# Performance work log

Measured on AMD Instinct MI355X. Metric: run time of the kernel, lower is better.

The kernel has to match this reference:

```python
import jax, jax.numpy as jnp
import numpy as np

D_MODEL = 1024
D_FF = 2048
NUM_EXPERTS = 16
TOP_K = 2
CAPACITY_FACTOR = 1.25
BATCH, SEQ = 4, 2048


def setup_inputs() -> dict:
    key = jax.random.key(0)
    k0, k1, k2, k3 = jax.random.split(key, 4)
    x = jax.random.normal(k0, (BATCH, SEQ, D_MODEL), jnp.float32)
    gate_w = jax.random.normal(k1, (NUM_EXPERTS, D_MODEL), jnp.float32) / np.float32(np.sqrt(D_MODEL))
    w1 = jax.random.normal(k2, (NUM_EXPERTS, D_MODEL, D_FF), jnp.float32) / np.float32(np.sqrt(D_MODEL))
    w2 = jax.random.normal(k3, (NUM_EXPERTS, D_FF, D_MODEL), jnp.float32) / np.float32(np.sqrt(D_FF))
    return {"x": x, "gate_w": gate_w, "w1": w1, "w2": w2}


def reference(x, gate_w, w1, w2):
    B, S, d = x.shape
    T = B * S
    E, K = NUM_EXPERTS, TOP_K
    capacity = int(CAPACITY_FACTOR * T * K / E)  # static

    xf = x.reshape(T, d)                                  # [T, d]
    logits = xf @ gate_w.T                                # [T, E]
    probs = jax.nn.sigmoid(logits)
    top_vals, sel = jax.lax.top_k(probs, K)               # [T, K]
    weights = top_vals / (top_vals.sum(-1, keepdims=True) + 1e-6)

    # Capacity-based ranking: rank of each (token, slot) within its expert,
    # in flattened token-major order (matches torch cumsum over one-hot).
    flat_sel = sel.reshape(-1)                            # [T*K]
    onehot = jax.nn.one_hot(flat_sel, E, dtype=jnp.int32)
    ranks = jnp.take_along_axis(jnp.cumsum(onehot, axis=0), flat_sel[:, None], axis=1)[:, 0] - 1
    valid = ranks < capacity                              # [T*K]

    sentinel = E * capacity
    slot = jnp.where(valid, flat_sel * capacity + ranks, sentinel)

    # token-major repeat matches x_flat.unsqueeze(1).expand(-1,K,-1).reshape(-1,d)
    x_rep = jnp.repeat(xf, K, axis=0)                     # [T*K, d]
    padded = jnp.zeros((sentinel + 1, d), xf.dtype).at[slot].set(x_rep)
    padded = padded[:sentinel].reshape(E, capacity, d)    # [E, C, d]

    h = jax.nn.gelu(jnp.einsum('ecd,edf->ecf', padded, w1), approximate=False)
    out_padded = jnp.einsum('ecf,efd->ecd', h, w2).reshape(sentinel, d)

    gathered = out_padded[jnp.minimum(slot, sentinel - 1)]
    gathered = jnp.where(valid[:, None], gathered, jnp.zeros((), xf.dtype))
    out = (gathered * weights.reshape(-1)[:, None]).reshape(T, K, d).sum(axis=1)
    return out.reshape(B, S, d)
```

## Files before the change

kernel.cpp:

```cpp
#include <hip/hip_runtime.h>
#include <math.h>

#define T_TOK 8192
#define DM 1024
#define DF 2048
#define NE 16
#define TK 2
#define CAP 1280

typedef __bf16 bf16x8 __attribute__((ext_vector_type(8)));
typedef float f32x4 __attribute__((ext_vector_type(4)));

__device__ __forceinline__ unsigned short f2bf(float f) {
  unsigned int u = __float_as_uint(f);
  unsigned int r = (u + 0x7fffu + ((u >> 16) & 1u)) >> 16;
  return (unsigned short)r;
}

__device__ __forceinline__ void async_copy16(const void* g, void* l) {
  __builtin_amdgcn_global_load_lds(
      (const __attribute__((address_space(1))) void*)g,
      (__attribute__((address_space(3))) void*)l, 16, 0, 0);
}

__global__ __launch_bounds__(256) void transpose_conv_kernel(
    const float* __restrict__ in, unsigned short* __restrict__ out, int R, int Cc) {
  __shared__ float tl[32][33];
  size_t eoff = (size_t)blockIdx.z * R * Cc;
  in += eoff; out += eoff;
  int c0 = blockIdx.x * 32, r0 = blockIdx.y * 32;
  int tx = threadIdx.x, ty = threadIdx.y;
#pragma unroll
  for (int r = 0; r < 4; r++)
    tl[ty + r * 8][tx] = in[(size_t)(r0 + ty + r * 8) * Cc + c0 + tx];
  __syncthreads();
#pragma unroll
  for (int r = 0; r < 4; r++)
    out[(size_t)(c0 + ty + r * 8) * R + r0 + tx] = f2bf(tl[tx][ty + r * 8]);
}

__global__ __launch_bounds__(64) void gate_kernel(
    const float* __restrict__ x, const float* __restrict__ gw,
    int* __restrict__ sel, float* __restrict__ wts) {
  int t = blockIdx.x;
  int lane = threadIdx.x;
  const float* xr = x + (size_t)t * DM;
  float acc[NE];
#pragma unroll
  for (int e = 0; e < NE; e++) acc[e] = 0.f;
  for (int j = 0; j < DM / 64; j++) {
    float xv = xr[j * 64 + lane];
#pragma unroll
    for (int e = 0; e < NE; e++) acc[e] += xv * gw[e * DM + j * 64 + lane];
  }
#pragma unroll
  for (int e = 0; e < NE; e++) {
    float v = acc[e];
#pragma unroll
    for (int off = 32; off > 0; off >>= 1) v += __shfl_xor(v, off);
    acc[e] = v;
  }
  if (lane == 0) {
    float p[NE];
#pragma unroll
    for (int e = 0; e < NE; e++) p[e] = 1.f / (1.f + expf(-acc[e]));
    int i0 = 0;
#pragma unroll
    for (int e = 1; e < NE; e++) if (p[e] > p[i0]) i0 = e;
    int i1 = (i0 == 0) ? 1 : 0;
#pragma unroll
    for (int e = 0; e < NE; e++) if (e != i0 && p[e] > p[i1]) i1 = e;
    float v0 = p[i0], v1 = p[i1], s = v0 + v1 + 1e-6f;
    sel[2 * t] = i0; sel[2 * t + 1] = i1;
    wts[2 * t] = v0 / s; wts[2 * t + 1] = v1 / s;
  }
}

__global__ __launch_bounds__(256) void scan_kernel(
    const int* __restrict__ sel, int* __restrict__ pos_slot,
    int* __restrict__ exp_tok, int* __restrict__ counts) {
  int e = blockIdx.x;
  __shared__ int wsum[4];
  int tid = threadIdx.x, lane = tid & 63, wv = tid >> 6;
  int base = 0;
  for (int p0 = 0; p0 < T_TOK * TK; p0 += 256) {
    int p = p0 + tid;
    int flag = (sel[p] == e) ? 1 : 0;
    unsigned long long b = __ballot(flag);
    int pre = __popcll(b & ((1ull << lane) - 1ull));
    if (lane == 0) wsum[wv] = __popcll(b);
    __syncthreads();
    int wbase = 0;
#pragma unroll
    for (int i = 0; i < 4; i++) if (i < wv) wbase += wsum[i];
    int tot = wsum[0] + wsum[1] + wsum[2] + wsum[3];
    if (flag) {
      int rank = base + wbase + pre;
      if (rank < CAP) {
        pos_slot[p] = e * CAP + rank;
        exp_tok[e * CAP + rank] = p;
      } else {
        pos_slot[p] = -1;
      }
    }
    base += tot;
    __syncthreads();
  }
  if (tid == 0) counts[e] = base < CAP ? base : CAP;
}

__global__ __launch_bounds__(128) void gather_kernel(
    const float* __restrict__ x, const int* __restrict__ exp_tok,
    const int* __restrict__ counts, unsigned short* __restrict__ Xp) {
  int i = blockIdx.x, e = blockIdx.y;
  int tid = threadIdx.x;
  unsigned short* dst = Xp + ((size_t)e * CAP + i) * DM;
  int4 pk = make_int4(0, 0, 0, 0);
  if (i < counts[e]) {
    int p = exp_tok[e * CAP + i];
    int t = p >> 1;
    const float4* src = (const float4*)(x + (size_t)t * DM);
    float4 v0 = src[tid * 2];
    float4 v1 = src[tid * 2 + 1];
    union { unsigned short u[8]; int4 v; } q;
    q.u[0] = f2bf(v0.x); q.u[1] = f2bf(v0.y); q.u[2] = f2bf(v0.z); q.u[3] = f2bf(v0.w);
    q.u[4] = f2bf(v1.x); q.u[5] = f2bf(v1.y); q.u[6] = f2bf(v1.z); q.u[7] = f2bf(v1.w);
    pk = q.v;
  }
  ((int4*)dst)[tid] = pk;
}

__device__ __forceinline__ void storev(unsigned short* p, float v) { *p = f2bf(v); }
__device__ __forceinline__ void storev(float* p, float v) { *p = v; }

template <bool GELU, typename OutT>
__global__ __launch_bounds__(256) void gemm_bt_kernel(
    const unsigned short* __restrict__ A, const unsigned short* __restrict__ Bt,
    OutT* __restrict__ C, int M, int N, int K,
    size_t sA, size_t sB, size_t sC) {
  __shared__ unsigned short As[128 * 32];
  __shared__ unsigned short Bs[128 * 32];
  A += (size_t)blockIdx.z * sA;
  Bt += (size_t)blockIdx.z * sB;
  C += (size_t)blockIdx.z * sC;
  int m0 = blockIdx.y * 128, n0 = blockIdx.x * 128;
  int tid = threadIdx.x;
  int lane = tid & 63;
  int wv = tid >> 6;
  int wm = (wv >> 1) * 64, wn = (wv & 1) * 64;
  int qd = lane >> 4, lm = lane & 15;

  const unsigned short* a0 = A + (size_t)(m0 + (tid >> 2)) * K + (tid & 3) * 8;
  const unsigned short* a1 = a0 + (size_t)64 * K;
  const unsigned short* b0 = Bt + (size_t)(n0 + (tid >> 2)) * K + (tid & 3) * 8;
  const unsigned short* b1 = b0 + (size_t)64 * K;
  char* lAs = (char*)As;
  char* lBs = (char*)Bs;

  f32x4 acc[4][4] = {};
  for (int k0 = 0; k0 < K; k0 += 32) {
    __syncthreads();
    async_copy16(a0 + k0, lAs + tid * 16);
    async_copy16(a1 + k0, lAs + (tid + 256) * 16);
    async_copy16(b0 + k0, lBs + tid * 16);
    async_copy16(b1 + k0, lBs + (tid + 256) * 16);
    __syncthreads();
    bf16x8 af[4], bfr[4];
#pragma unroll
    for (int i = 0; i < 4; i++)
      af[i] = *(const bf16x8*)(lAs + (wm + i * 16 + lm) * 64 + qd * 16);
#pragma unroll
    for (int j = 0; j < 4; j++)
      bfr[j] = *(const bf16x8*)(lBs + (wn + j * 16 + lm) * 64 + qd * 16);
#pragma unroll
    for (int i = 0; i < 4; i++)
#pragma unroll
      for (int j = 0; j < 4; j++)
        acc[i][j] = __builtin_amdgcn_mfma_f32_16x16x32_bf16(af[i], bfr[j], acc[i][j], 0, 0, 0);
  }
#pragma unroll
  for (int i = 0; i < 4; i++) {
    int row = m0 + wm + i * 16 + qd * 4;
#pragma unroll
    for (int j = 0; j < 4; j++) {
      int col = n0 + wn + j * 16 + lm;
#pragma unroll
      for (int r = 0; r < 4; r++) {
        float v = acc[i][j][r];
        if (GELU) v = 0.5f * v * (1.f + erff(v * 0.70710678118f));
        storev(&C[(size_t)(row + r) * N + col], v);
      }
    }
  }
}

__global__ __launch_bounds__(128) void combine_kernel(
    const float* __restrict__ outp, const int* __restrict__ pos_slot,
    const float* __restrict__ wts, float* __restrict__ out) {
  int t = blockIdx.x, tid = threadIdx.x;
  float4 r0 = make_float4(0.f, 0.f, 0.f, 0.f);
  float4 r1 = make_float4(0.f, 0.f, 0.f, 0.f);
#pragma unroll
  for (int k = 0; k < 2; k++) {
    int p = 2 * t + k;
    int s = pos_slot[p];
    if (s >= 0) {
      float w = wts[p];
      const float4* src = (const float4*)(outp + (size_t)s * DM);
      float4 a = src[tid * 2], b = src[tid * 2 + 1];
      r0.x += w * a.x; r0.y += w * a.y; r0.z += w * a.z; r0.w += w * a.w;
      r1.x += w * b.x; r1.y += w * b.y; r1.z += w * b.z; r1.w += w * b.w;
    }
  }
  float4* dst = (float4*)(out + (size_t)t * DM);
  dst[tid * 2] = r0;
  dst[tid * 2 + 1] = r1;
}

extern "C" void kernel_launch(void* const* d_in, const int* in_sizes, int n_in,
                              void* d_out, int out_size, void* d_ws, size_t ws_size,
                              hipStream_t stream) {
  (void)in_sizes; (void)n_in; (void)out_size; (void)ws_size;
  const float* x  = (const float*)d_in[0];
  const float* gw = (const float*)d_in[1];
  const float* w1 = (const float*)d_in[2];
  const float* w2 = (const float*)d_in[3];
  float* out = (float*)d_out;

  char* ws = (char*)d_ws;
  unsigned short* w1t = (unsigned short*)ws; ws += (size_t)NE * DM * DF * 2;
  unsigned short* w2t = (unsigned short*)ws; ws += (size_t)NE * DF * DM * 2;
  unsigned short* Xp  = (unsigned short*)ws; ws += (size_t)NE * CAP * DM * 2;
  unsigned short* H   = (unsigned short*)ws; ws += (size_t)NE * CAP * DF * 2;
  float* outp = (float*)ws;  ws += (size_t)NE * CAP * DM * 4;
  int* sel = (int*)ws;       ws += (size_t)T_TOK * TK * 4;
  float* wts = (float*)ws;   ws += (size_t)T_TOK * TK * 4;
  int* pos_slot = (int*)ws;  ws += (size_t)T_TOK * TK * 4;
  int* exp_tok = (int*)ws;   ws += (size_t)NE * CAP * 4;
  int* counts = (int*)ws;    ws += (size_t)NE * 4;

  transpose_conv_kernel<<<dim3(DF / 32, DM / 32, NE), dim3(32, 8), 0, stream>>>(w1, w1t, DM, DF);
  transpose_conv_kernel<<<dim3(DM / 32, DF / 32, NE), dim3(32, 8), 0, stream>>>(w2, w2t, DF, DM);
  gate_kernel<<<T_TOK, 64, 0, stream>>>(x, gw, sel, wts);
  scan_kernel<<<NE, 256, 0, stream>>>(sel, pos_slot, exp_tok, counts);
  gather_kernel<<<dim3(CAP, NE), 128, 0, stream>>>(x, exp_tok, counts, Xp);
  gemm_bt_kernel<true, unsigned short><<<dim3(DF / 128, CAP / 128, NE), 256, 0, stream>>>(
      Xp, w1t, H, CAP, DF, DM, (size_t)CAP * DM, (size_t)DM * DF, (size_t)CAP * DF);
  gemm_bt_kernel<false, float><<<dim3(DM / 128, CAP / 128, NE), 256, 0, stream>>>(
      H, w2t, outp, CAP, DM, DF, (size_t)CAP * DF, (size_t)DF * DM, (size_t)CAP * DM);
  combine_kernel<<<T_TOK, 128, 0, stream>>>(outp, pos_slot, wts, out);
}
```

Baseline: 729.9 us.

## Fuse combine into second GEMM via atomics, swizzle LDS, vectorize transpose and gate

The second expert GEMM now scatters its weighted results straight into the output with atomicAdd, after a memset. This removes the fp32 padded output buffer, the pos_slot array and the separate combine kernel. Both GEMMs get an XOR swizzle on the LDS chunk index to cut bank conflicts. The weight transpose/convert kernel now uses 64x64 tiles with float4 loads and int4 stores, and the gate kernel caches gate weights in shared memory and handles four tokens per block. In exchange, the atomics make the output summation order nondeterministic and add contention on each output row.

```diff
diff --git a/kernel.cpp b/kernel.cpp
--- a/kernel.cpp
+++ b/kernel.cpp
@@ -25,33 +25,54 @@
 
 __global__ __launch_bounds__(256) void transpose_conv_kernel(
     const float* __restrict__ in, unsigned short* __restrict__ out, int R, int Cc) {
-  __shared__ float tl[32][33];
+  __shared__ unsigned short tl[64][72];
   size_t eoff = (size_t)blockIdx.z * R * Cc;
   in += eoff; out += eoff;
-  int c0 = blockIdx.x * 32, r0 = blockIdx.y * 32;
-  int tx = threadIdx.x, ty = threadIdx.y;
-#pragma unroll
-  for (int r = 0; r < 4; r++)
-    tl[ty + r * 8][tx] = in[(size_t)(r0 + ty + r * 8) * Cc + c0 + tx];
+  int c0 = blockIdx.x * 64, r0 = blockIdx.y * 64;
+  int t = threadIdx.x;
+#pragma unroll
+  for (int i = 0; i < 4; i++) {
+    int r = (t >> 4) + i * 16;
+    int c = (t & 15) * 4;
+    float4 v = *(const float4*)(in + (size_t)(r0 + r) * Cc + c0 + c);
+    tl[c + 0][r] = f2bf(v.x);
+    tl[c + 1][r] = f2bf(v.y);
+    tl[c + 2][r] = f2bf(v.z);
+    tl[c + 3][r] = f2bf(v.w);
+  }
   __syncthreads();
 #pragma unroll
-  for (int r = 0; r < 4; r++)
-    out[(size_t)(c0 + ty + r * 8) * R + r0 + tx] = f2bf(tl[tx][ty + r * 8]);
-}
-
-__global__ __launch_bounds__(64) void gate_kernel(
+  for (int i = 0; i < 2; i++) {
+    int c = (t >> 3) + i * 32;
+    int r = (t & 7) * 8;
+    *(int4*)(out + (size_t)(c0 + c) * R + r0 + r) = *(const int4*)&tl[c][r];
+  }
+}
+
+__global__ __launch_bounds__(256) void gate_kernel(
     const float* __restrict__ x, const float* __restrict__ gw,
     int* __restrict__ sel, float* __restrict__ wts) {
-  int t = blockIdx.x;
-  int lane = threadIdx.x;
-  const float* xr = x + (size_t)t * DM;
+  __shared__ float sgw[NE * DM];
+  int tid = threadIdx.x, lane = tid & 63, wv = tid >> 6;
+  for (int i = tid; i < NE * DM / 4; i += 256)
+    ((float4*)sgw)[i] = ((const float4*)gw)[i];
+  __syncthreads();
+  int t = blockIdx.x * 4 + wv;
+  const float4* xr = (const float4*)(x + (size_t)t * DM);
+  float4 xv[4];
+#pragma unroll
+  for (int j = 0; j < 4; j++) xv[j] = xr[j * 64 + lane];
+  const float4* g4 = (const float4*)sgw;
   float acc[NE];
 #pragma unroll
-  for (int e = 0; e < NE; e++) acc[e] = 0.f;
-  for (int j = 0; j < DM / 64; j++) {
-    float xv = xr[j * 64 + lane];
-#pragma unroll
-    for (int e = 0; e < NE; e++) acc[e] += xv * gw[e * DM + j * 64 + lane];
+  for (int e = 0; e < NE; e++) {
+    float s = 0.f;
+#pragma unroll
+    for (int j = 0; j < 4; j++) {
+      float4 g = g4[e * 256 + j * 64 + lane];
+      s += xv[j].x * g.x + xv[j].y * g.y + xv[j].z * g.z + xv[j].w * g.w;
+    }
+    acc[e] = s;
   }
 #pragma unroll
   for (int e = 0; e < NE; e++) {
@@ -77,8 +98,7 @@
 }
 
 __global__ __launch_bounds__(256) void scan_kernel(
-    const int* __restrict__ sel, int* __restrict__ pos_slot,
-    int* __restrict__ exp_tok, int* __restrict__ counts) {
+    const int* __restrict__ sel, int* __restrict__ exp_tok, int* __restrict__ counts) {
   int e = blockIdx.x;
   __shared__ int wsum[4];
   int tid = threadIdx.x, lane = tid & 63, wv = tid >> 6;
@@ -96,12 +116,7 @@
     int tot = wsum[0] + wsum[1] + wsum[2] + wsum[3];
     if (flag) {
       int rank = base + wbase + pre;
-      if (rank < CAP) {
-        pos_slot[p] = e * CAP + rank;
-        exp_tok[e * CAP + rank] = p;
-      } else {
-        pos_slot[p] = -1;
-      }
+      if (rank < CAP) exp_tok[e * CAP + rank] = p;
     }
     base += tot;
     __syncthreads();
@@ -130,13 +145,9 @@
   ((int4*)dst)[tid] = pk;
 }
 
-__device__ __forceinline__ void storev(unsigned short* p, float v) { *p = f2bf(v); }
-__device__ __forceinline__ void storev(float* p, float v) { *p = v; }
-
-template <bool GELU, typename OutT>
-__global__ __launch_bounds__(256) void gemm_bt_kernel(
+__global__ __launch_bounds__(256) void gemm1_kernel(
     const unsigned short* __restrict__ A, const unsigned short* __restrict__ Bt,
-    OutT* __restrict__ C, int M, int N, int K,
+    unsigned short* __restrict__ C, int M, int N, int K,
     size_t sA, size_t sB, size_t sC) {
   __shared__ unsigned short As[128 * 32];
   __shared__ unsigned short Bs[128 * 32];
@@ -149,10 +160,12 @@
   int wv = tid >> 6;
   int wm = (wv >> 1) * 64, wn = (wv & 1) * 64;
   int qd = lane >> 4, lm = lane & 15;
-
-  const unsigned short* a0 = A + (size_t)(m0 + (tid >> 2)) * K + (tid & 3) * 8;
+  int sa = (lm >> 1) & 3;
+  int chunk = (tid & 3) ^ ((tid >> 3) & 3);
+
+  const unsigned short* a0 = A + (size_t)(m0 + (tid >> 2)) * K + chunk * 8;
   const unsigned short* a1 = a0 + (size_t)64 * K;
-  const unsigned short* b0 = Bt + (size_t)(n0 + (tid >> 2)) * K + (tid & 3) * 8;
+  const unsigned short* b0 = Bt + (size_t)(n0 + (tid >> 2)) * K + chunk * 8;
   const unsigned short* b1 = b0 + (size_t)64 * K;
   char* lAs = (char*)As;
   char* lBs = (char*)Bs;
@@ -168,10 +181,10 @@
     bf16x8 af[4], bfr[4];
 #pragma unroll
     for (int i = 0; i < 4; i++)
-      af[i] = *(const bf16x8*)(lAs + (wm + i * 16 + lm) * 64 + qd * 16);
+      af[i] = *(const bf16x8*)(lAs + (wm + i * 16 + lm) * 64 + (qd ^ sa) * 16);
 #pragma unroll
     for (int j = 0; j < 4; j++)
-      bfr[j] = *(const bf16x8*)(lBs + (wn + j * 16 + lm) * 64 + qd * 16);
+      bfr[j] = *(const bf16x8*)(lBs + (wn + j * 16 + lm) * 64 + (qd ^ sa) * 16);
 #pragma unroll
     for (int i = 0; i < 4; i++)
 #pragma unroll
@@ -187,34 +200,79 @@
 #pragma unroll
       for (int r = 0; r < 4; r++) {
         float v = acc[i][j][r];
-        if (GELU) v = 0.5f * v * (1.f + erff(v * 0.70710678118f));
-        storev(&C[(size_t)(row + r) * N + col], v);
+        v = 0.5f * v * (1.f + erff(v * 0.70710678118f));
+        C[(size_t)(row + r) * N + col] = f2bf(v);
       }
     }
   }
 }
 
-__global__ __launch_bounds__(128) void combine_kernel(
-    const float* __restrict__ outp, const int* __restrict__ pos_slot,
-    const float* __restrict__ wts, float* __restrict__ out) {
-  int t = blockIdx.x, tid = threadIdx.x;
-  float4 r0 = make_float4(0.f, 0.f, 0.f, 0.f);
-  float4 r1 = make_float4(0.f, 0.f, 0.f, 0.f);
-#pragma unroll
-  for (int k = 0; k < 2; k++) {
-    int p = 2 * t + k;
-    int s = pos_slot[p];
-    if (s >= 0) {
-      float w = wts[p];
-      const float4* src = (const float4*)(outp + (size_t)s * DM);
-      float4 a = src[tid * 2], b = src[tid * 2 + 1];
-      r0.x += w * a.x; r0.y += w * a.y; r0.z += w * a.z; r0.w += w * a.w;
-      r1.x += w * b.x; r1.y += w * b.y; r1.z += w * b.z; r1.w += w * b.w;
+__global__ __launch_bounds__(256) void gemm2_kernel(
+    const unsigned short* __restrict__ A, const unsigned short* __restrict__ Bt,
+    float* __restrict__ out, const int* __restrict__ exp_tok,
+    const int* __restrict__ counts, const float* __restrict__ wts,
+    int M, int N, int K, size_t sA, size_t sB) {
+  __shared__ unsigned short As[128 * 32];
+  __shared__ unsigned short Bs[128 * 32];
+  int e = blockIdx.z;
+  A += (size_t)e * sA;
+  Bt += (size_t)e * sB;
+  int m0 = blockIdx.y * 128, n0 = blockIdx.x * 128;
+  int tid = threadIdx.x;
+  int lane = tid & 63;
+  int wv = tid >> 6;
+  int wm = (wv >> 1) * 64, wn = (wv & 1) * 64;
+  int qd = lane >> 4, lm = lane & 15;
+  int sa = (lm >> 1) & 3;
+  int chunk = (tid & 3) ^ ((tid >> 3) & 3);
+
+  const unsigned short* a0 = A + (size_t)(m0 + (tid >> 2)) * K + chunk * 8;
+  const unsigned short* a1 = a0 + (size_t)64 * K;
+  const unsigned short* b0 = Bt + (size_t)(n0 + (tid >> 2)) * K + chunk * 8;
+  const unsigned short* b1 = b0 + (size_t)64 * K;
+  char* lAs = (char*)As;
+  char* lBs = (char*)Bs;
+
+  f32x4 acc[4][4] = {};
+  for (int k0 = 0; k0 < K; k0 += 32) {
+    __syncthreads();
+    async_copy16(a0 + k0, lAs + tid * 16);
+    async_copy16(a1 + k0, lAs + (tid + 256) * 16);
+    async_copy16(b0 + k0, lBs + tid * 16);
+    async_copy16(b1 + k0, lBs + (tid + 256) * 16);
+    __syncthreads();
+    bf16x8 af[4], bfr[4];
+#pragma unroll
+    for (int i = 0; i < 4; i++)
+      af[i] = *(const bf16x8*)(lAs + (wm + i * 16 + lm) * 64 + (qd ^ sa) * 16);
+#pragma unroll
+    for (int j = 0; j < 4; j++)
+      bfr[j] = *(const bf16x8*)(lBs + (wn + j * 16 + lm) * 64 + (qd ^ sa) * 16);
+#pragma unroll
+    for (int i = 0; i < 4; i++)
+#pragma unroll
+      for (int j = 0; j < 4; j++)
+        acc[i][j] = __builtin_amdgcn_mfma_f32_16x16x32_bf16(af[i], bfr[j], acc[i][j], 0, 0, 0);
+  }
+  int cnt = counts[e];
+#pragma unroll
+  for (int i = 0; i < 4; i++) {
+    int base_row = m0 + wm + i * 16 + qd * 4;
+#pragma unroll
+    for (int r = 0; r < 4; r++) {
+      int slot = base_row + r;
+      if (slot < cnt) {
+        int p = exp_tok[e * CAP + slot];
+        float w = wts[p];
+        float* orow = out + (size_t)(p >> 1) * DM;
+#pragma unroll
+        for (int j = 0; j < 4; j++) {
+          int col = n0 + wn + j * 16 + lm;
+          atomicAdd(orow + col, w * acc[i][j][r]);
+        }
+      }
     }
   }
-  float4* dst = (float4*)(out + (size_t)t * DM);
-  dst[tid * 2] = r0;
-  dst[tid * 2 + 1] = r1;
 }
 
 extern "C" void kernel_launch(void* const* d_in, const int* in_sizes, int n_in,
@@ -232,21 +290,20 @@
   unsigned short* w2t = (unsigned short*)ws; ws += (size_t)NE * DF * DM * 2;
   unsigned short* Xp  = (unsigned short*)ws; ws += (size_t)NE * CAP * DM * 2;
   unsigned short* H   = (unsigned short*)ws; ws += (size_t)NE * CAP * DF * 2;
-  float* outp = (float*)ws;  ws += (size_t)NE * CAP * DM * 4;
   int* sel = (int*)ws;       ws += (size_t)T_TOK * TK * 4;
   float* wts = (float*)ws;   ws += (size_t)T_TOK * TK * 4;
-  int* pos_slot = (int*)ws;  ws += (size_t)T_TOK * TK * 4;
   int* exp_tok = (int*)ws;   ws += (size_t)NE * CAP * 4;
   int* counts = (int*)ws;    ws += (size_t)NE * 4;
 
-  transpose_conv_kernel<<<dim3(DF / 32, DM / 32, NE), dim3(32, 8), 0, stream>>>(w1, w1t, DM, DF);
-  transpose_conv_kernel<<<dim3(DM / 32, DF / 32, NE), dim3(32, 8), 0, stream>>>(w2, w2t, DF, DM);
-  gate_kernel<<<T_TOK, 64, 0, stream>>>(x, gw, sel, wts);
-  scan_kernel<<<NE, 256, 0, stream>>>(sel, pos_slot, exp_tok, counts);
+  hipMemsetAsync(out, 0, (size_t)T_TOK * DM * 4, stream);
+
+  transpose_conv_kernel<<<dim3(DF / 64, DM / 64, NE), 256, 0, stream>>>(w1, w1t, DM, DF);
+  transpose_conv_kernel<<<dim3(DM / 64, DF / 64, NE), 256, 0, stream>>>(w2, w2t, DF, DM);
+  gate_kernel<<<T_TOK / 4, 256, 0, stream>>>(x, gw, sel, wts);
+  scan_kernel<<<NE, 256, 0, stream>>>(sel, exp_tok, counts);
   gather_kernel<<<dim3(CAP, NE), 128, 0, stream>>>(x, exp_tok, counts, Xp);
-  gemm_bt_kernel<true, unsigned short><<<dim3(DF / 128, CAP / 128, NE), 256, 0, stream>>>(
+  gemm1_kernel<<<dim3(DF / 128, CAP / 128, NE), 256, 0, stream>>>(
       Xp, w1t, H, CAP, DF, DM, (size_t)CAP * DM, (size_t)DM * DF, (size_t)CAP * DF);
-  gemm_bt_kernel<false, float><<<dim3(DM / 128, CAP / 128, NE), 256, 0, stream>>>(
-      H, w2t, outp, CAP, DM, DF, (size_t)CAP * DF, (size_t)DF * DM, (size_t)CAP * DM);
-  combine_kernel<<<T_TOK, 128, 0, stream>>>(outp, pos_slot, wts, out);
-}
+  gemm2_kernel<<<dim3(DM / 128, CAP / 128, NE), 256, 0, stream>>>(
+      H, w2t, out, exp_tok, counts, wts, CAP, DM, DF, (size_t)CAP * DF, (size_t)DF * DM);
+}
```

Result: slower. 747.9 us (+2.5%).
